# Kernel tuning notes

Measured on AMD Instinct MI355X. Metric: run time of the kernel, lower is better.

## Reference

```python
import jax, jax.numpy as jnp
import numpy as np

# ---- static structure (from LastFMModel source) ----
COUNTS = (50000, 80000, 10000)   # user, item, tag node counts
FEAT, HID, INTRA, INTER = 256, 128, 64, 128
E = 500000                        # edges per metapath hop
# hops listed leaf->target as (src_type, dst_type, edge_type)
MP_USER = [[(0, 1, 0), (1, 0, 1)],
           [(0, 1, 0), (1, 2, 2), (2, 1, 3), (1, 0, 1)],
           [(0, 0, 4)]]
MP_ITEM = [[(1, 0, 1), (0, 1, 0)],
           [(1, 2, 2), (2, 1, 3)],
           [(1, 0, 1), (0, 0, 4), (0, 1, 0)]]
# get_gcn_encoder: etype in {1,2,4} -> encoder 1, {0,3} -> encoder 2
GCN_GROUP = {0: 2, 1: 1, 2: 1, 3: 2, 4: 1}
OFFSETS = (0, COUNTS[0], COUNTS[0] + COUNTS[1])


def _gen_edges(mps, rng):
    rows = []
    for hops in mps:
        for (st, dt, et) in hops:
            rows.append(np.stack([rng.integers(0, COUNTS[st], E),
                                  rng.integers(0, COUNTS[dt], E)]))
    return jnp.asarray(np.stack(rows), jnp.int32)


def setup_inputs() -> dict:
    rng = np.random.default_rng(0)
    ks = jax.random.split(jax.random.key(0), 16)
    n_total = sum(COUNTS)
    s = 0.05
    d = {}
    d['features'] = jax.random.normal(ks[0], (n_total, FEAT), jnp.float32)
    d['edges_user'] = _gen_edges(MP_USER, rng)
    d['edges_item'] = _gen_edges(MP_ITEM, rng)
    d['perm_user'] = jnp.asarray(rng.permutation(COUNTS[0]), jnp.int32)
    d['perm_item'] = jnp.asarray(rng.permutation(COUNTS[1]), jnp.int32)
    d['W_type'] = jax.random.normal(ks[1], (3, FEAT, HID), jnp.float32) * s
    d['b_type'] = jnp.zeros((3, HID), jnp.float32)
    d['comp_vec'] = jax.random.normal(ks[2], (5, HID), jnp.float32) * s
    d['W_gcn'] = jax.random.normal(ks[3], (3, HID, HID), jnp.float32) * s
    d['b_gcn'] = jnp.zeros((3, HID), jnp.float32)
    d['fc_u'] = jax.random.normal(ks[4], (3, HID, INTRA), jnp.float32) * s
    d['fcr_u'] = jax.random.normal(ks[5], (3, INTRA, HID), jnp.float32) * s
    d['V_u'] = jax.random.normal(ks[6], (3 * INTRA, INTER), jnp.float32) * s
    d['Vr_u'] = jax.random.normal(ks[7], (INTER, 3 * INTRA), jnp.float32) * s
    d['fc_i'] = jax.random.normal(ks[8], (3, HID, INTRA), jnp.float32) * s
    d['fcr_i'] = jax.random.normal(ks[9], (3, INTRA, HID), jnp.float32) * s
    d['V_i'] = jax.random.normal(ks[10], (3 * INTRA, INTER), jnp.float32) * s
    d['Vr_i'] = jax.random.normal(ks[11], (INTER, 3 * INTRA), jnp.float32) * s
    return d


def _propagate(h_src, src, dst, etype, n_dst, comp_vec, W_gcn, b_gcn):
    # CompGCN composition (elementwise) + GraphConv norm='right' (in-degree mean)
    msg = h_src[src] * comp_vec[etype]                                  # [E, HID]
    agg = jax.ops.segment_sum(msg, dst, num_segments=n_dst)
    deg = jax.ops.segment_sum(jnp.ones_like(dst, jnp.float32), dst, num_segments=n_dst)
    h = agg / jnp.clip(deg, 1.0)[:, None]
    g = GCN_GROUP[etype]
    return h @ W_gcn[g] + b_gcn[g]


def _fusion(outs, fc, fcr, V, Vr):
    # AutoMvFusion: per-view intra projection, shared inter fusion,
    # reconstruction loss + pairwise view orthogonality loss
    z_list = [jnp.tanh(h @ fc[p]) for p, h in enumerate(outs)]          # [N, INTRA] each
    z = jnp.concatenate(z_list, axis=1)                                 # [N, 3*INTRA]
    fused = z @ V                                                       # [N, INTER]
    z_rec = fused @ Vr
    re = jnp.float32(0.0)
    for p, h in enumerate(outs):
        h_rec = z_rec[:, p * INTRA:(p + 1) * INTRA] @ fcr[p]
        re = re + jnp.mean((h_rec - h) ** 2)
    orth = jnp.float32(0.0)
    for p in range(3):
        for q in range(p + 1, 3):
            g = z_list[p].T @ z_list[q]                                 # [INTRA, INTRA]
            orth = orth + jnp.mean(g ** 2)
    return fused, re + orth


def _run_layer(mp_hops, edges, perm, t_feats, comp_vec, W_gcn, b_gcn, fc, fcr, V, Vr):
    k = 0
    outs = []
    for hops in mp_hops:
        h = t_feats[hops[0][0]]           # leaf-type transformed features
        for (st, dt, et) in hops:
            h = _propagate(h, edges[k, 0], edges[k, 1], et, COUNTS[dt],
                           comp_vec, W_gcn, b_gcn)
            k += 1
        outs.append(h[perm])              # new_index_arrangement reindex
    return _fusion(outs, fc, fcr, V, Vr)


def reference(features, edges_user, edges_item, perm_user, perm_item,
              W_type, b_type, comp_vec, W_gcn, b_gcn,
              fc_u, fcr_u, V_u, Vr_u, fc_i, fcr_i, V_i, Vr_i):
    # NodeTransform: per-type linear + activation (dropout off at eval)
    t_feats = [jax.nn.relu(features[OFFSETS[t]:OFFSETS[t] + COUNTS[t]] @ W_type[t] + b_type[t])
               for t in range(3)]
    h_user, loss_u = _run_layer(MP_USER, edges_user, perm_user, t_feats,
                                comp_vec, W_gcn, b_gcn, fc_u, fcr_u, V_u, Vr_u)
    h_item, loss_i = _run_layer(MP_ITEM, edges_item, perm_item, t_feats,
                                comp_vec, W_gcn, b_gcn, fc_i, fcr_i, V_i, Vr_i)
    return h_user, h_item, loss_u + loss_i
```

## Files before the change

### kernel.cpp

```cpp
#include <hip/hip_runtime.h>

typedef unsigned short u16;
typedef unsigned int   u32;

#define ACT_NONE 0
#define ACT_RELU 1
#define ACT_TANH 2

#define E_EDGES 500000
#define RP_STRIDE 80004
#define NCH 62
#define CH 8192
#define HSTRIDE 19456

using s8vec = __attribute__((ext_vector_type(8))) short;
using f4vec = __attribute__((ext_vector_type(4))) float;

__device__ __forceinline__ float bf2f(u16 u) {
  union { u32 b; float f; } v; v.b = ((u32)u) << 16; return v.f;
}
__device__ __forceinline__ u16 f2bf(float x) {
  union { float f; u32 b; } v; v.f = x;
  u32 r = v.b + 0x7fffu + ((v.b >> 16) & 1u);
  return (u16)(r >> 16);
}
__device__ __forceinline__ void acc8(float* acc, uint4 v) {
  union { u32 b; float f; } cv;
  cv.b = v.x << 16;         acc[0] += cv.f;
  cv.b = v.x & 0xffff0000u; acc[1] += cv.f;
  cv.b = v.y << 16;         acc[2] += cv.f;
  cv.b = v.y & 0xffff0000u; acc[3] += cv.f;
  cv.b = v.z << 16;         acc[4] += cv.f;
  cv.b = v.z & 0xffff0000u; acc[5] += cv.f;
  cv.b = v.w << 16;         acc[6] += cv.f;
  cv.b = v.w & 0xffff0000u; acc[7] += cv.f;
}

struct TJob { const float* src; u16* dst; const float* scale; int R; int C; };
struct TBatch { TJob j[24]; };
__global__ __launch_bounds__(256) void transpose_b_k(TBatch b) {
  TJob jb = b.j[blockIdx.y];
  int i = blockIdx.x * 256 + threadIdx.x;
  if (i >= jb.R * jb.C) return;
  int r = i / jb.C, c = i % jb.C;
  float v = jb.src[i];
  if (jb.scale) v *= jb.scale[r];
  jb.dst[(size_t)c * jb.R + r] = f2bf(v);
}

struct IBatch { const int* perm[2]; int* ip[2]; int n[2]; };
__global__ __launch_bounds__(256) void iperm_b_k(IBatch b) {
  int y = blockIdx.y;
  int i = blockIdx.x * 256 + threadIdx.x;
  if (i < b.n[y]) b.ip[y][b.perm[y][i]] = i;
}

struct CsrP { int n[14]; int sh[14]; int P[14]; };

__global__ __launch_bounds__(256) void csr_hist_k(
    const int* __restrict__ eu, const int* __restrict__ ei,
    int* __restrict__ hista, CsrP cp) {
  const int hop = blockIdx.y, chunk = blockIdx.x;
  const int P = cp.P[hop], sh = cp.sh[hop];
  __shared__ int hist[320];
  for (int i = threadIdx.x; i < P; i += 256) hist[i] = 0;
  __syncthreads();
  const int* edges = (hop < 7) ? eu : ei;
  const int h7 = (hop < 7) ? hop : hop - 7;
  const int* dstp = edges + (size_t)(h7 * 2 + 1) * E_EDGES;
  const int e0 = chunk * CH;
  const int e1 = min(E_EDGES, e0 + CH);
  for (int e = e0 + threadIdx.x * 4; e < e1; e += 1024) {
    int4 d4 = *(const int4*)(dstp + e);
    atomicAdd(&hist[d4.x >> sh], 1);
    atomicAdd(&hist[d4.y >> sh], 1);
    atomicAdd(&hist[d4.z >> sh], 1);
    atomicAdd(&hist[d4.w >> sh], 1);
  }
  __syncthreads();
  for (int i = threadIdx.x; i < P; i += 256)
    hista[(size_t)hop * HSTRIDE + i * NCH + chunk] = hist[i];
}

__global__ __launch_bounds__(256) void csr_scan_k(int* __restrict__ hista, CsrP cp) {
  const int hop = blockIdx.x;
  const int L = cp.P[hop] * NCH;
  int* a = hista + (size_t)hop * HSTRIDE;
  const int per = (L + 255) >> 8;
  const int lo = threadIdx.x * per;
  const int hi = min(L, lo + per);
  int s = 0;
  for (int i = lo; i < hi; ++i) s += a[i];
  __shared__ int lds[256];
  lds[threadIdx.x] = s;
  __syncthreads();
  for (int off = 1; off < 256; off <<= 1) {
    int v = (threadIdx.x >= off) ? lds[threadIdx.x - off] : 0;
    __syncthreads();
    lds[threadIdx.x] += v;
    __syncthreads();
  }
  int run = threadIdx.x ? lds[threadIdx.x - 1] : 0;
  for (int i = lo; i < hi; ++i) { int v = a[i]; a[i] = run; run += v; }
}

__global__ __launch_bounds__(256) void csr_scatter_k(
    const int* __restrict__ eu, const int* __restrict__ ei,
    const int* __restrict__ hista, u32* __restrict__ bp, CsrP cp) {
  const int hop = blockIdx.y, chunk = blockIdx.x;
  const int P = cp.P[hop], sh = cp.sh[hop];
  const u32 fm = (1u << sh) - 1u;
  __shared__ int cur[320];
  for (int i = threadIdx.x; i < P; i += 256)
    cur[i] = hista[(size_t)hop * HSTRIDE + i * NCH + chunk];
  __syncthreads();
  const int* edges = (hop < 7) ? eu : ei;
  const int h7 = (hop < 7) ? hop : hop - 7;
  const int* srcp = edges + (size_t)(h7 * 2) * E_EDGES;
  const int* dstp = srcp + E_EDGES;
  u32* b = bp + (size_t)hop * E_EDGES;
  const int e0 = chunk * CH;
  const int e1 = min(E_EDGES, e0 + CH);
  for (int e = e0 + threadIdx.x * 4; e < e1; e += 1024) {
    int4 d4 = *(const int4*)(dstp + e);
    int4 s4 = *(const int4*)(srcp + e);
    int dd[4] = {d4.x, d4.y, d4.z, d4.w};
    int ss[4] = {s4.x, s4.y, s4.z, s4.w};
#pragma unroll
    for (int j = 0; j < 4; ++j) {
      int pos = atomicAdd(&cur[dd[j] >> sh], 1);
      b[pos] = (u32)ss[j] | (((u32)dd[j] & fm) << 24);
    }
  }
}

__global__ __launch_bounds__(256) void csr_fine_k(
    const u32* __restrict__ bp, const int* __restrict__ hista,
    int* __restrict__ rowptrb, int* __restrict__ esrcb, CsrP cp) {
  const int hop = blockIdx.y, p = blockIdx.x;
  const int P = cp.P[hop];
  if (p >= P) return;
  const int n = cp.n[hop], sh = cp.sh[hop], W = 1 << sh;
  const int* fl = hista + (size_t)hop * HSTRIDE;
  const int beg = fl[p * NCH];
  const int end = (p + 1 < P) ? fl[(p + 1) * NCH] : E_EDGES;
  const int nb = min(W, n - p * W);
  const int tid = threadIdx.x;

  __shared__ int fh[256];
  __shared__ int sc[256];
  __shared__ int cur[256];
  fh[tid] = 0;
  __syncthreads();
  const u32* b = bp + (size_t)hop * E_EDGES;
  for (int i = beg + tid; i < end; i += 256)
    atomicAdd(&fh[b[i] >> 24], 1);
  __syncthreads();
  sc[tid] = fh[tid];
  __syncthreads();
  for (int off = 1; off < 256; off <<= 1) {
    int v = (tid >= off) ? sc[tid - off] : 0;
    __syncthreads();
    sc[tid] += v;
    __syncthreads();
  }
  const int excl = tid ? sc[tid - 1] : 0;
  int* rowptr = rowptrb + (size_t)hop * RP_STRIDE;
  if (tid < nb) rowptr[p * W + tid] = beg + excl;
  cur[tid] = beg + excl;
  if (p == P - 1 && tid == 0) rowptr[n] = E_EDGES;
  __syncthreads();
  int* esrc = esrcb + (size_t)hop * E_EDGES;
  for (int i = beg + tid; i < end; i += 256) {
    u32 v = b[i];
    int pos = atomicAdd(&cur[v >> 24], 1);
    esrc[pos] = (int)(v & 0xFFFFFFu);
  }
}

struct HopJob {
  const u16* h; const int* rowptr; const int* esrc;
  const u16* Bt; const float* bias; u16* out;
  const int* iperm; int n; int permout;
};
struct HopBatch { HopJob j[6]; };

__global__ __launch_bounds__(512) void hop_b_k(HopBatch batch) {
  const HopJob jb = batch.j[blockIdx.y];
  const int rbase = blockIdx.x * 128;
  if (rbase >= jb.n) return;

  __shared__ u16 bts[128 * 128];
  const int tid = threadIdx.x;
  for (int i = tid; i < 128 * 16; i += 512) {
    int nn = i >> 4, g = i & 15;
    int gs = (g & 8) | ((g ^ nn) & 7);
    *(uint4*)(&bts[nn * 128 + gs * 8]) = *(const uint4*)(jb.Bt + (size_t)nn * 128 + g * 8);
  }
  __syncthreads();

  const int wave = tid >> 6;
  const int lane = tid & 63;
  const int kgrp = lane >> 4;
  const int lid  = lane & 15;
  const int d = rbase + wave * 16 + lid;

  float a0[8] = {0,0,0,0,0,0,0,0}, a1[8] = {0,0,0,0,0,0,0,0};
  float a2[8] = {0,0,0,0,0,0,0,0}, a3[8] = {0,0,0,0,0,0,0,0};
  int s0 = 0, s1 = 0;
  if (d < jb.n) { s0 = jb.rowptr[d]; s1 = jb.rowptr[d + 1]; }
  const u16* hk = jb.h + kgrp * 8;
  int i = s0;
  for (; i + 3 < s1; i += 4) {
    int ea = jb.esrc[i], eb = jb.esrc[i + 1], ec = jb.esrc[i + 2], ed = jb.esrc[i + 3];
    const u16* ra = hk + (size_t)ea * 128;
    const u16* rb = hk + (size_t)eb * 128;
    const u16* rc = hk + (size_t)ec * 128;
    const u16* rd = hk + (size_t)ed * 128;
    uint4 va0 = *(const uint4*)(ra);      uint4 vb0 = *(const uint4*)(rb);
    uint4 vc0 = *(const uint4*)(rc);      uint4 vd0 = *(const uint4*)(rd);
    uint4 va1 = *(const uint4*)(ra + 32); uint4 vb1 = *(const uint4*)(rb + 32);
    uint4 vc1 = *(const uint4*)(rc + 32); uint4 vd1 = *(const uint4*)(rd + 32);
    uint4 va2 = *(const uint4*)(ra + 64); uint4 vb2 = *(const uint4*)(rb + 64);
    uint4 vc2 = *(const uint4*)(rc + 64); uint4 vd2 = *(const uint4*)(rd + 64);
    uint4 va3 = *(const uint4*)(ra + 96); uint4 vb3 = *(const uint4*)(rb + 96);
    uint4 vc3 = *(const uint4*)(rc + 96); uint4 vd3 = *(const uint4*)(rd + 96);
    acc8(a0, va0); acc8(a0, vb0); acc8(a0, vc0); acc8(a0, vd0);
    acc8(a1, va1); acc8(a1, vb1); acc8(a1, vc1); acc8(a1, vd1);
    acc8(a2, va2); acc8(a2, vb2); acc8(a2, vc2); acc8(a2, vd2);
    acc8(a3, va3); acc8(a3, vb3); acc8(a3, vc3); acc8(a3, vd3);
  }
  for (; i + 1 < s1; i += 2) {
    const u16* ra = hk + (size_t)jb.esrc[i] * 128;
    const u16* rb = hk + (size_t)jb.esrc[i + 1] * 128;
    uint4 va0 = *(const uint4*)(ra);      uint4 vb0 = *(const uint4*)(rb);
    uint4 va1 = *(const uint4*)(ra + 32); uint4 vb1 = *(const uint4*)(rb + 32);
    uint4 va2 = *(const uint4*)(ra + 64); uint4 vb2 = *(const uint4*)(rb + 64);
    uint4 va3 = *(const uint4*)(ra + 96); uint4 vb3 = *(const uint4*)(rb + 96);
    acc8(a0, va0); acc8(a1, va1); acc8(a2, va2); acc8(a3, va3);
    acc8(a0, vb0); acc8(a1, vb1); acc8(a2, vb2); acc8(a3, vb3);
  }
  if (i < s1) {
    const u16* ra = hk + (size_t)jb.esrc[i] * 128;
    acc8(a0, *(const uint4*)(ra));
    acc8(a1, *(const uint4*)(ra + 32));
    acc8(a2, *(const uint4*)(ra + 64));
    acc8(a3, *(const uint4*)(ra + 96));
  }
  const float rs = 1.0f / fmaxf((float)(s1 - s0), 1.0f);
  s8vec f0, f1, f2, f3;
#pragma unroll
  for (int j = 0; j < 8; ++j) f0[j] = (short)f2bf(a0[j] * rs);
#pragma unroll
  for (int j = 0; j < 8; ++j) f1[j] = (short)f2bf(a1[j] * rs);
#pragma unroll
  for (int j = 0; j < 8; ++j) f2[j] = (short)f2bf(a2[j] * rs);
#pragma unroll
  for (int j = 0; j < 8; ++j) f3[j] = (short)f2bf(a3[j] * rs);

#pragma unroll
  for (int t = 0; t < 8; ++t) {
    f4vec c = {0.f, 0.f, 0.f, 0.f};
    const int bn = t * 16 + lid;
    int g = kgrp;
    int gs = (g & 8) | ((g ^ bn) & 7);
    c = __builtin_amdgcn_mfma_f32_16x16x32_bf16(f0, *(const s8vec*)(&bts[bn * 128 + gs * 8]), c, 0, 0, 0);
    g = 4 + kgrp; gs = (g & 8) | ((g ^ bn) & 7);
    c = __builtin_amdgcn_mfma_f32_16x16x32_bf16(f1, *(const s8vec*)(&bts[bn * 128 + gs * 8]), c, 0, 0, 0);
    g = 8 + kgrp; gs = (g & 8) | ((g ^ bn) & 7);
    c = __builtin_amdgcn_mfma_f32_16x16x32_bf16(f2, *(const s8vec*)(&bts[bn * 128 + gs * 8]), c, 0, 0, 0);
    g = 12 + kgrp; gs = (g & 8) | ((g ^ bn) & 7);
    c = __builtin_amdgcn_mfma_f32_16x16x32_bf16(f3, *(const s8vec*)(&bts[bn * 128 + gs * 8]), c, 0, 0, 0);
    const int col = bn;
    const float bb = jb.bias[col];
#pragma unroll
    for (int j = 0; j < 4; ++j) {
      int r = rbase + wave * 16 + kgrp * 4 + j;
      if (r < jb.n) {
        float v = c[j] + bb;
        int ro = jb.permout ? jb.iperm[r] : r;
        jb.out[(size_t)ro * 128 + col] = f2bf(v);
      }
    }
  }
}

struct GemmJob {
  const void* A; const u16* Bt; const float* bias; void* C;
  const u16* target; float* loss; u16* Ct; int M;
};
struct GemmBatch { GemmJob j[3]; };

template <int K, int N, int ACT, int AMODE, bool CF32, bool SQDIFF, bool CTR>
__global__ __launch_bounds__(256) void gemm_b_k(
    GemmBatch batch, int ldA, int ldC, int ldCt) {
  static_assert(K % 32 == 0 && N % 16 == 0, "");
  const GemmJob jb = batch.j[blockIdx.y];
  const int rbase0 = blockIdx.x * 64;
  if (rbase0 >= jb.M) return;

  __shared__ u16 bts[N * K];
  __shared__ float red[4];

  const int tid = threadIdx.x;
  for (int i = tid; i < N * (K / 8); i += 256) {
    int n = i / (K / 8);
    int g = i % (K / 8);
    int gs = (g & ~7) | ((g ^ n) & 7);
    *(uint4*)(&bts[n * K + gs * 8]) = *(const uint4*)(jb.Bt + (size_t)n * K + g * 8);
  }
  __syncthreads();

  const int wave = tid >> 6;
  const int lane = tid & 63;
  const int kgrp = lane >> 4;
  const int rbase = rbase0 + wave * 16;
  const int rowA = rbase + (lane & 15);
  const bool av = rowA < jb.M;

  s8vec afr[K / 32];
  if constexpr (AMODE == 1) {
    const float* arow = (const float*)jb.A + (size_t)rowA * ldA;
#pragma unroll
    for (int kt = 0; kt < K / 32; ++kt) {
      s8vec fr = {0, 0, 0, 0, 0, 0, 0, 0};
      if (av) {
        const float* p = arow + kt * 32 + kgrp * 8;
        float4 fa = *(const float4*)(p);
        float4 fb = *(const float4*)(p + 4);
        fr[0] = (short)f2bf(fa.x); fr[1] = (short)f2bf(fa.y);
        fr[2] = (short)f2bf(fa.z); fr[3] = (short)f2bf(fa.w);
        fr[4] = (short)f2bf(fb.x); fr[5] = (short)f2bf(fb.y);
        fr[6] = (short)f2bf(fb.z); fr[7] = (short)f2bf(fb.w);
      }
      afr[kt] = fr;
    }
  } else {
    const u16* arow = (const u16*)jb.A + (size_t)rowA * ldA;
#pragma unroll
    for (int kt = 0; kt < K / 32; ++kt) {
      s8vec fr = {0, 0, 0, 0, 0, 0, 0, 0};
      if (av) fr = *(const s8vec*)(arow + kt * 32 + kgrp * 8);
      afr[kt] = fr;
    }
  }

  float sqsum = 0.0f;
#pragma unroll
  for (int t = 0; t < N / 16; ++t) {
    f4vec acc = {0.f, 0.f, 0.f, 0.f};
    const int bn = t * 16 + (lane & 15);
#pragma unroll
    for (int kt = 0; kt < K / 32; ++kt) {
      int g = kt * 4 + kgrp;
      int gs = (g & ~7) | ((g ^ bn) & 7);
      s8vec bfr = *(const s8vec*)(&bts[bn * K + gs * 8]);
      acc = __builtin_amdgcn_mfma_f32_16x16x32_bf16(afr[kt], bfr, acc, 0, 0, 0);
    }
    const int col = t * 16 + (lane & 15);
    float bb = jb.bias ? jb.bias[col] : 0.0f;
#pragma unroll
    for (int j = 0; j < 4; ++j) {
      int r = rbase + kgrp * 4 + j;
      if (r < jb.M) {
        float v = acc[j] + bb;
        if constexpr (ACT == ACT_RELU) v = fmaxf(v, 0.0f);
        if constexpr (ACT == ACT_TANH) v = tanhf(v);
        if constexpr (SQDIFF) {
          float dd = v - bf2f(jb.target[(size_t)r * N + col]);
          sqsum += dd * dd;
        } else if constexpr (CF32) {
          ((float*)jb.C)[(size_t)r * ldC + col] = v;
        } else {
          ((u16*)jb.C)[(size_t)r * ldC + col] = f2bf(v);
        }
        if constexpr (CTR) {
          jb.Ct[(size_t)col * ldCt + r] = f2bf(v);
        }
      }
    }
  }

  if constexpr (SQDIFF) {
#pragma unroll
    for (int off = 32; off > 0; off >>= 1) sqsum += __shfl_down(sqsum, off);
    if (lane == 0) red[wave] = sqsum;
    __syncthreads();
    if (tid == 0) atomicAdd(jb.loss, red[0] + red[1] + red[2] + red[3]);
  }
}

#define GRAM_NKB 40
__global__ __launch_bounds__(256) void gram_k(
    const u16* __restrict__ zt, int NP, float* __restrict__ G3) {
  const int pair = blockIdx.y;
  const int p = (pair == 2) ? 1 : 0;
  const int q = (pair == 0) ? 1 : 2;
  const int wave = threadIdx.x >> 6;
  const int lane = threadIdx.x & 63;
  const int kgrp = lane >> 4, lid = lane & 15;

  const int KC = (((NP + GRAM_NKB - 1) / GRAM_NKB) + 31) & ~31;
  const int kbeg = blockIdx.x * KC;
  const int kend = min(NP, kbeg + KC);

  const u16* arow = zt + (size_t)(p * 64 + wave * 16 + lid) * NP;
  const u16* brow0 = zt + (size_t)(q * 64 + 0 * 16 + lid) * NP;
  const u16* brow1 = zt + (size_t)(q * 64 + 1 * 16 + lid) * NP;
  const u16* brow2 = zt + (size_t)(q * 64 + 2 * 16 + lid) * NP;
  const u16* brow3 = zt + (size_t)(q * 64 + 3 * 16 + lid) * NP;

  f4vec acc0 = {0.f, 0.f, 0.f, 0.f};
  f4vec acc1 = {0.f, 0.f, 0.f, 0.f};
  f4vec acc2 = {0.f, 0.f, 0.f, 0.f};
  f4vec acc3 = {0.f, 0.f, 0.f, 0.f};

  for (int k0 = kbeg; k0 < kend; k0 += 32) {
    const int ko = k0 + kgrp * 8;
    s8vec af = *(const s8vec*)(arow + ko);
    s8vec b0 = *(const s8vec*)(brow0 + ko);
    s8vec b1 = *(const s8vec*)(brow1 + ko);
    s8vec b2 = *(const s8vec*)(brow2 + ko);
    s8vec b3 = *(const s8vec*)(brow3 + ko);
    acc0 = __builtin_amdgcn_mfma_f32_16x16x32_bf16(af, b0, acc0, 0, 0, 0);
    acc1 = __builtin_amdgcn_mfma_f32_16x16x32_bf16(af, b1, acc1, 0, 0, 0);
    acc2 = __builtin_amdgcn_mfma_f32_16x16x32_bf16(af, b2, acc2, 0, 0, 0);
    acc3 = __builtin_amdgcn_mfma_f32_16x16x32_bf16(af, b3, acc3, 0, 0, 0);
  }

  float* g = G3 + (size_t)pair * 4096;
  const int mrow = wave * 16 + kgrp * 4;
#pragma unroll
  for (int j = 0; j < 4; ++j) {
    atomicAdd(&g[(mrow + j) * 64 + 0 * 16 + lid], acc0[j]);
    atomicAdd(&g[(mrow + j) * 64 + 1 * 16 + lid], acc1[j]);
    atomicAdd(&g[(mrow + j) * 64 + 2 * 16 + lid], acc2[j]);
    atomicAdd(&g[(mrow + j) * 64 + 3 * 16 + lid], acc3[j]);
  }
}

__global__ __launch_bounds__(256) void loss_k(
    const float* __restrict__ G, const float* __restrict__ RE,
    float* __restrict__ out) {
  float s = 0.f;
  for (int i = threadIdx.x; i < 2 * 3 * 4096; i += 256) { float g = G[i]; s += g * g; }
#pragma unroll
  for (int off = 32; off > 0; off >>= 1) s += __shfl_down(s, off);
  __shared__ float red[4];
  int wave = threadIdx.x >> 6, lane = threadIdx.x & 63;
  if (lane == 0) red[wave] = s;
  __syncthreads();
  if (threadIdx.x == 0) {
    float orth = (red[0] + red[1] + red[2] + red[3]) / 4096.0f;
    float loss = orth + RE[0] / (50000.0f * 128.0f) + RE[1] / (80000.0f * 128.0f);
    out[0] = loss;
  }
}

static const int COUNTS_H[3] = {50000, 80000, 10000};
static const int OFFS_H[3]   = {0, 50000, 130000};
static const int GRP_H[5]    = {2, 1, 1, 2, 1};
static const int HOPN[14] = {80000, 50000, 80000, 10000, 80000, 50000, 50000,
                             50000, 80000, 10000, 80000, 50000, 50000, 80000};

extern "C" void kernel_launch(void* const* d_in, const int* in_sizes, int n_in,
                              void* d_out, int out_size, void* d_ws, size_t ws_size,
                              hipStream_t stream) {
  (void)in_sizes; (void)n_in; (void)out_size; (void)ws_size;

  const float* features = (const float*)d_in[0];
  const int* e_user   = (const int*)d_in[1];
  const int* e_item   = (const int*)d_in[2];
  const int* perm_u   = (const int*)d_in[3];
  const int* perm_i   = (const int*)d_in[4];
  const float* W_type = (const float*)d_in[5];
  const float* b_type = (const float*)d_in[6];
  const float* comp   = (const float*)d_in[7];
  const float* W_gcn  = (const float*)d_in[8];
  const float* b_gcn  = (const float*)d_in[9];
  const float* fc[2]  = {(const float*)d_in[10], (const float*)d_in[14]};
  const float* fcr[2] = {(const float*)d_in[11], (const float*)d_in[15]};
  const float* V[2]   = {(const float*)d_in[12], (const float*)d_in[16]};
  const float* Vr[2]  = {(const float*)d_in[13], (const float*)d_in[17]};
  float* out = (float*)d_out;

  char* base = (char*)d_ws;
  size_t off = 0;
  auto alloc = [&](size_t b) -> void* {
    void* p = base + off;
    off = (off + b + 255) & ~(size_t)255;
    return p;
  };
  u16* TF    = (u16*)alloc(140000ull * 128 * 2);
  u16* HB    = (u16*)alloc(330000ull * 128 * 2);
  u16* OUTSu = (u16*)alloc(3ull * 50000 * 128 * 2);
  u16* OUTSi = (u16*)alloc(3ull * 80000 * 128 * 2);
  int* HISTA    = (int*)alloc(14ull * HSTRIDE * 4);
  int* ROWPTR14 = (int*)alloc(14ull * RP_STRIDE * 4);
  int* ESRC14   = (int*)alloc(14ull * E_EDGES * 4);
  int* IPERM    = (int*)alloc(130000ull * 4);
  u16* WT_TYPE = (u16*)alloc(3ull * 128 * 256 * 2);
  u16* BT_HOP  = (u16*)alloc(5ull * 128 * 128 * 2);
  u16* FCT     = (u16*)alloc(6ull * 64 * 128 * 2);
  u16* VT      = (u16*)alloc(2ull * 128 * 192 * 2);
  u16* VRT     = (u16*)alloc(2ull * 192 * 128 * 2);
  u16* FCRT    = (u16*)alloc(6ull * 128 * 64 * 2);
  float* G   = (float*)alloc((2 * 3 * 4096 + 2) * 4);
  float* RE  = G + 2 * 3 * 4096;

  u32* BP   = (u32*)HB;
  u16* Z    = HB;
  u16* ZREC = HB + 80000ull * 192;
  u16* ZT   = (u16*)HISTA;

  const int hbrow[7] = {0, 80000, 160000, 170000, 220000, 230000, 280000};
  auto HBp = [&](int c) { return HB + (size_t)hbrow[c] * 128; };
  auto RP  = [&](int g) { return ROWPTR14 + (size_t)g * RP_STRIDE; };
  auto ES  = [&](int g) { return ESRC14 + (size_t)g * E_EDGES; };
  auto BT  = [&](int et) { return BT_HOP + (size_t)et * 128 * 128; };
  auto BG  = [&](int et) { return b_gcn + (size_t)GRP_H[et] * 128; };

  TBatch tb;
  int tj = 0;
  for (int t = 0; t < 3; ++t)
    tb.j[tj++] = {W_type + (size_t)t * 256 * 128, WT_TYPE + (size_t)t * 128 * 256, nullptr, 256, 128};
  for (int et = 0; et < 5; ++et)
    tb.j[tj++] = {W_gcn + (size_t)GRP_H[et] * 128 * 128, BT_HOP + (size_t)et * 128 * 128,
                  comp + (size_t)et * 128, 128, 128};
  for (int L = 0; L < 2; ++L)
    for (int p = 0; p < 3; ++p)
      tb.j[tj++] = {fc[L] + (size_t)p * 128 * 64, FCT + (size_t)(L * 3 + p) * 64 * 128, nullptr, 128, 64};
  for (int L = 0; L < 2; ++L)
    for (int p = 0; p < 3; ++p)
      tb.j[tj++] = {fcr[L] + (size_t)p * 64 * 128, FCRT + (size_t)(L * 3 + p) * 128 * 64, nullptr, 64, 128};
  for (int L = 0; L < 2; ++L)
    tb.j[tj++] = {V[L], VT + (size_t)L * 128 * 192, nullptr, 192, 128};
  for (int L = 0; L < 2; ++L)
    tb.j[tj++] = {Vr[L], VRT + (size_t)L * 192 * 128, nullptr, 128, 192};
  transpose_b_k<<<dim3(128, 24), 256, 0, stream>>>(tb);

  IBatch ib;
  ib.perm[0] = perm_u; ib.ip[0] = IPERM;          ib.n[0] = 50000;
  ib.perm[1] = perm_i; ib.ip[1] = IPERM + 50000;  ib.n[1] = 80000;
  iperm_b_k<<<dim3(313, 2), 256, 0, stream>>>(ib);

  CsrP cpp;
  for (int g = 0; g < 14; ++g) {
    cpp.n[g] = HOPN[g];
    cpp.sh[g] = (HOPN[g] <= 10000) ? 6 : 8;
    cpp.P[g] = (HOPN[g] + (1 << cpp.sh[g]) - 1) >> cpp.sh[g];
  }
  csr_hist_k<<<dim3(NCH, 14), 256, 0, stream>>>(e_user, e_item, HISTA, cpp);
  csr_scan_k<<<dim3(14), 256, 0, stream>>>(HISTA, cpp);
  csr_scatter_k<<<dim3(NCH, 14), 256, 0, stream>>>(e_user, e_item, HISTA, BP, cpp);
  csr_fine_k<<<dim3(313, 14), 256, 0, stream>>>(BP, HISTA, ROWPTR14, ESRC14, cpp);
  hipMemsetAsync(G, 0, (2 * 3 * 4096 + 2) * 4, stream);

  {
    GemmBatch nb;
    for (int t = 0; t < 3; ++t)
      nb.j[t] = {features + (size_t)OFFS_H[t] * 256, WT_TYPE + (size_t)t * 128 * 256,
                 b_type + (size_t)t * 128, TF + (size_t)OFFS_H[t] * 128,
                 nullptr, nullptr, nullptr, COUNTS_H[t]};
    gemm_b_k<256, 128, ACT_RELU, 1, false, false, false>
        <<<dim3(1250, 3), 256, 0, stream>>>(nb, 256, 128, 0);
  }

  const u16* TF0 = TF;
  const u16* TF1 = TF + 50000ull * 128;
  const int* IPu = IPERM;
  const int* IPi = IPERM + 50000;

  HopBatch L0, L1, L2, L3;
  L0.j[0] = {TF0, RP(0),  ES(0),  BT(0), BG(0), HBp(0), nullptr, 80000, 0};
  L0.j[1] = {TF0, RP(2),  ES(2),  BT(0), BG(0), HBp(1), nullptr, 80000, 0};
  L0.j[2] = {TF0, RP(6),  ES(6),  BT(4), BG(4), OUTSu + 2ull * 50000 * 128, IPu, 50000, 1};
  L0.j[3] = {TF1, RP(7),  ES(7),  BT(1), BG(1), HBp(3), nullptr, 50000, 0};
  L0.j[4] = {TF1, RP(9),  ES(9),  BT(2), BG(2), HBp(4), nullptr, 10000, 0};
  L0.j[5] = {TF1, RP(11), ES(11), BT(1), BG(1), HBp(5), nullptr, 50000, 0};
  L1.j[0] = {HBp(0), RP(1),  ES(1),  BT(1), BG(1), OUTSu, IPu, 50000, 1};
  L1.j[1] = {HBp(1), RP(3),  ES(3),  BT(2), BG(2), HBp(2), nullptr, 10000, 0};
  L1.j[2] = {HBp(3), RP(8),  ES(8),  BT(0), BG(0), OUTSi, IPi, 80000, 1};
  L1.j[3] = {HBp(4), RP(10), ES(10), BT(3), BG(3), OUTSi + 1ull * 80000 * 128, IPi, 80000, 1};
  L1.j[4] = {HBp(5), RP(12), ES(12), BT(4), BG(4), HBp(6), nullptr, 50000, 0};
  L1.j[5] = L1.j[4];
  L2.j[0] = {HBp(2), RP(4),  ES(4),  BT(3), BG(3), HBp(0), nullptr, 80000, 0};
  L2.j[1] = {HBp(6), RP(13), ES(13), BT(0), BG(0), OUTSi + 2ull * 80000 * 128, IPi, 80000, 1};
  L2.j[2] = L2.j[1]; L2.j[3] = L2.j[1]; L2.j[4] = L2.j[1]; L2.j[5] = L2.j[1];
  L3.j[0] = {HBp(0), RP(5), ES(5), BT(1), BG(1), OUTSu + 1ull * 50000 * 128, IPu, 50000, 1};
  L3.j[1] = L3.j[0]; L3.j[2] = L3.j[0]; L3.j[3] = L3.j[0]; L3.j[4] = L3.j[0]; L3.j[5] = L3.j[0];

  hop_b_k<<<dim3(625, 6), 512, 0, stream>>>(L0);
  hop_b_k<<<dim3(625, 5), 512, 0, stream>>>(L1);
  hop_b_k<<<dim3(625, 2), 512, 0, stream>>>(L2);
  hop_b_k<<<dim3(391, 1), 512, 0, stream>>>(L3);

  for (int L = 0; L < 2; ++L) {
    const int nL = L ? 80000 : 50000;
    const int NP = (nL + 31) & ~31;
    u16* OUTS_L = L ? OUTSi : OUTSu;
    const size_t pstride = (size_t)nL * 128;
    const dim3 gg((unsigned)((nL + 63) / 64));

    if (NP != nL)
      hipMemsetAsync(ZT, 0, (size_t)192 * NP * 2, stream);

    GemmBatch fb;
    for (int p = 0; p < 3; ++p)
      fb.j[p] = {OUTS_L + p * pstride, FCT + (size_t)(L * 3 + p) * 64 * 128, nullptr,
                 Z + p * 64, nullptr, nullptr, ZT + (size_t)p * 64 * NP, nL};
    gemm_b_k<128, 64, ACT_TANH, 0, false, false, true>
        <<<dim3(gg.x, 3), 256, 0, stream>>>(fb, 128, 192, NP);

    gram_k<<<dim3(GRAM_NKB, 3), 256, 0, stream>>>(ZT, NP, G + (size_t)L * 3 * 4096);

    float* fused = out + (L ? 6400000 : 0);
    GemmBatch vb;
    vb.j[0] = {Z, VT + (size_t)L * 128 * 192, nullptr, fused, nullptr, nullptr, nullptr, nL};
    vb.j[1] = vb.j[0]; vb.j[2] = vb.j[0];
    gemm_b_k<192, 128, ACT_NONE, 0, true, false, false>
        <<<dim3(gg.x, 1), 256, 0, stream>>>(vb, 192, 128, 0);

    GemmBatch rb;
    rb.j[0] = {fused, VRT + (size_t)L * 192 * 128, nullptr, ZREC, nullptr, nullptr, nullptr, nL};
    rb.j[1] = rb.j[0]; rb.j[2] = rb.j[0];
    gemm_b_k<128, 192, ACT_NONE, 1, false, false, false>
        <<<dim3(gg.x, 1), 256, 0, stream>>>(rb, 128, 192, 0);

    GemmBatch sb;
    for (int p = 0; p < 3; ++p)
      sb.j[p] = {ZREC + p * 64, FCRT + (size_t)(L * 3 + p) * 128 * 64, nullptr,
                 nullptr, OUTS_L + p * pstride, RE + L, nullptr, nL};
    gemm_b_k<64, 128, ACT_NONE, 0, false, true, false>
        <<<dim3(gg.x, 3), 256, 0, stream>>>(sb, 192, 0, 0);
  }

  loss_k<<<1, 256, 0, stream>>>(G, RE, out + 16640000);
}
```

Before: 1.119 ms.

## Sort destination rows by degree to balance hop aggregation, shrink hop blocks

Adds three kernels that build a per-hop permutation of destination rows bucketed by in-degree (counting sort over degrees capped at 63). The hop gather kernel now handles rows in that order, so the 16 lanes sharing a wave have similar edge counts and lanes spend less time idle on divergent loop trip counts. Output rows are remapped through the sort, and the hop block shrinks from 512 to 256 threads with 64 rows per block and more blocks. The cost is extra preprocessing launches, an indirect row lookup, and scattered output writes with less locality.

```diff
diff --git a/kernel.cpp b/kernel.cpp
--- a/kernel.cpp
+++ b/kernel.cpp
@@ -12,6 +12,9 @@
 #define NCH 62
 #define CH 8192
 #define HSTRIDE 19456
+#define DCH 2048
+#define DNCH 40
+#define DH_STRIDE (64 * DNCH)
 
 using s8vec = __attribute__((ext_vector_type(8))) short;
 using f4vec = __attribute__((ext_vector_type(4))) float;
@@ -178,21 +181,79 @@
   }
 }
 
+__global__ __launch_bounds__(256) void deg_hist_k(
+    const int* __restrict__ rowptrb, int* __restrict__ dh, CsrP cp) {
+  const int hop = blockIdx.y, ch = blockIdx.x;
+  const int n = cp.n[hop];
+  __shared__ int h[64];
+  if (threadIdx.x < 64) h[threadIdx.x] = 0;
+  __syncthreads();
+  const int* rp = rowptrb + (size_t)hop * RP_STRIDE;
+  const int d0 = ch * DCH;
+  const int d1 = min(n, d0 + DCH);
+  for (int d = d0 + threadIdx.x; d < d1; d += 256)
+    atomicAdd(&h[min(rp[d + 1] - rp[d], 63)], 1);
+  __syncthreads();
+  if (threadIdx.x < 64)
+    dh[(size_t)hop * DH_STRIDE + threadIdx.x * DNCH + ch] = h[threadIdx.x];
+}
+
+__global__ __launch_bounds__(256) void deg_scan_k(int* __restrict__ dh) {
+  int* a = dh + (size_t)blockIdx.x * DH_STRIDE;
+  const int L = DH_STRIDE;
+  const int per = (L + 255) >> 8;
+  const int lo = threadIdx.x * per;
+  const int hi = min(L, lo + per);
+  int s = 0;
+  for (int i = lo; i < hi; ++i) s += a[i];
+  __shared__ int lds[256];
+  lds[threadIdx.x] = s;
+  __syncthreads();
+  for (int off = 1; off < 256; off <<= 1) {
+    int v = (threadIdx.x >= off) ? lds[threadIdx.x - off] : 0;
+    __syncthreads();
+    lds[threadIdx.x] += v;
+    __syncthreads();
+  }
+  int run = threadIdx.x ? lds[threadIdx.x - 1] : 0;
+  for (int i = lo; i < hi; ++i) { int v = a[i]; a[i] = run; run += v; }
+}
+
+__global__ __launch_bounds__(256) void deg_scatter_k(
+    const int* __restrict__ rowptrb, const int* __restrict__ dh,
+    int* __restrict__ dsortb, CsrP cp) {
+  const int hop = blockIdx.y, ch = blockIdx.x;
+  const int n = cp.n[hop];
+  const int d0 = ch * DCH;
+  if (d0 >= n) return;
+  __shared__ int cur[64];
+  if (threadIdx.x < 64)
+    cur[threadIdx.x] = dh[(size_t)hop * DH_STRIDE + threadIdx.x * DNCH + ch];
+  __syncthreads();
+  const int* rp = rowptrb + (size_t)hop * RP_STRIDE;
+  int* ds = dsortb + (size_t)hop * RP_STRIDE;
+  const int d1 = min(n, d0 + DCH);
+  for (int d = d0 + threadIdx.x; d < d1; d += 256) {
+    int pos = atomicAdd(&cur[min(rp[d + 1] - rp[d], 63)], 1);
+    ds[pos] = d;
+  }
+}
+
 struct HopJob {
-  const u16* h; const int* rowptr; const int* esrc;
+  const u16* h; const int* rowptr; const int* esrc; const int* dsort;
   const u16* Bt; const float* bias; u16* out;
   const int* iperm; int n; int permout;
 };
 struct HopBatch { HopJob j[6]; };
 
-__global__ __launch_bounds__(512) void hop_b_k(HopBatch batch) {
+__global__ __launch_bounds__(256, 4) void hop_b_k(HopBatch batch) {
   const HopJob jb = batch.j[blockIdx.y];
-  const int rbase = blockIdx.x * 128;
+  const int rbase = blockIdx.x * 64;
   if (rbase >= jb.n) return;
 
   __shared__ u16 bts[128 * 128];
   const int tid = threadIdx.x;
-  for (int i = tid; i < 128 * 16; i += 512) {
+  for (int i = tid; i < 128 * 16; i += 256) {
     int nn = i >> 4, g = i & 15;
     int gs = (g & 8) | ((g ^ nn) & 7);
     *(uint4*)(&bts[nn * 128 + gs * 8]) = *(const uint4*)(jb.Bt + (size_t)nn * 128 + g * 8);
@@ -203,12 +264,16 @@
   const int lane = tid & 63;
   const int kgrp = lane >> 4;
   const int lid  = lane & 15;
-  const int d = rbase + wave * 16 + lid;
+  const int dv = rbase + wave * 16 + lid;
 
   float a0[8] = {0,0,0,0,0,0,0,0}, a1[8] = {0,0,0,0,0,0,0,0};
   float a2[8] = {0,0,0,0,0,0,0,0}, a3[8] = {0,0,0,0,0,0,0,0};
   int s0 = 0, s1 = 0;
-  if (d < jb.n) { s0 = jb.rowptr[d]; s1 = jb.rowptr[d + 1]; }
+  if (dv < jb.n) {
+    int d = jb.dsort[dv];
+    s0 = jb.rowptr[d];
+    s1 = jb.rowptr[d + 1];
+  }
   const u16* hk = jb.h + kgrp * 8;
   int i = s0;
   for (; i + 3 < s1; i += 4) {
@@ -258,6 +323,18 @@
 #pragma unroll
   for (int j = 0; j < 8; ++j) f3[j] = (short)f2bf(a3[j] * rs);
 
+  int rout[4];
+#pragma unroll
+  for (int j = 0; j < 4; ++j) {
+    int rv = rbase + wave * 16 + kgrp * 4 + j;
+    if (rv < jb.n) {
+      int rr = jb.dsort[rv];
+      rout[j] = jb.permout ? jb.iperm[rr] : rr;
+    } else {
+      rout[j] = -1;
+    }
+  }
+
 #pragma unroll
   for (int t = 0; t < 8; ++t) {
     f4vec c = {0.f, 0.f, 0.f, 0.f};
@@ -275,11 +352,9 @@
     const float bb = jb.bias[col];
 #pragma unroll
     for (int j = 0; j < 4; ++j) {
-      int r = rbase + wave * 16 + kgrp * 4 + j;
-      if (r < jb.n) {
+      if (rout[j] >= 0) {
         float v = c[j] + bb;
-        int ro = jb.permout ? jb.iperm[r] : r;
-        jb.out[(size_t)ro * 128 + col] = f2bf(v);
+        jb.out[(size_t)rout[j] * 128 + col] = f2bf(v);
       }
     }
   }
@@ -498,6 +573,8 @@
   int* HISTA    = (int*)alloc(14ull * HSTRIDE * 4);
   int* ROWPTR14 = (int*)alloc(14ull * RP_STRIDE * 4);
   int* ESRC14   = (int*)alloc(14ull * E_EDGES * 4);
+  int* DSORT14  = (int*)alloc(14ull * RP_STRIDE * 4);
+  int* DH       = (int*)alloc(14ull * DH_STRIDE * 4);
   int* IPERM    = (int*)alloc(130000ull * 4);
   u16* WT_TYPE = (u16*)alloc(3ull * 128 * 256 * 2);
   u16* BT_HOP  = (u16*)alloc(5ull * 128 * 128 * 2);
@@ -517,6 +594,7 @@
   auto HBp = [&](int c) { return HB + (size_t)hbrow[c] * 128; };
   auto RP  = [&](int g) { return ROWPTR14 + (size_t)g * RP_STRIDE; };
   auto ES  = [&](int g) { return ESRC14 + (size_t)g * E_EDGES; };
+  auto DS  = [&](int g) { return DSORT14 + (size_t)g * RP_STRIDE; };
   auto BT  = [&](int et) { return BT_HOP + (size_t)et * 128 * 128; };
   auto BG  = [&](int et) { return b_gcn + (size_t)GRP_H[et] * 128; };
 
@@ -554,6 +632,10 @@
   csr_scan_k<<<dim3(14), 256, 0, stream>>>(HISTA, cpp);
   csr_scatter_k<<<dim3(NCH, 14), 256, 0, stream>>>(e_user, e_item, HISTA, BP, cpp);
   csr_fine_k<<<dim3(313, 14), 256, 0, stream>>>(BP, HISTA, ROWPTR14, ESRC14, cpp);
+
+  deg_hist_k<<<dim3(DNCH, 14), 256, 0, stream>>>(ROWPTR14, DH, cpp);
+  deg_scan_k<<<dim3(14), 256, 0, stream>>>(DH);
+  deg_scatter_k<<<dim3(DNCH, 14), 256, 0, stream>>>(ROWPTR14, DH, DSORT14, cpp);
   hipMemsetAsync(G, 0, (2 * 3 * 4096 + 2) * 4, stream);
 
   {
@@ -572,28 +654,28 @@
   const int* IPi = IPERM + 50000;
 
   HopBatch L0, L1, L2, L3;
-  L0.j[0] = {TF0, RP(0),  ES(0),  BT(0), BG(0), HBp(0), nullptr, 80000, 0};
-  L0.j[1] = {TF0, RP(2),  ES(2),  BT(0), BG(0), HBp(1), nullptr, 80000, 0};
-  L0.j[2] = {TF0, RP(6),  ES(6),  BT(4), BG(4), OUTSu + 2ull * 50000 * 128, IPu, 50000, 1};
-  L0.j[3] = {TF1, RP(7),  ES(7),  BT(1), BG(1), HBp(3), nullptr, 50000, 0};
-  L0.j[4] = {TF1, RP(9),  ES(9),  BT(2), BG(2), HBp(4), nullptr, 10000, 0};
-  L0.j[5] = {TF1, RP(11), ES(11), BT(1), BG(1), HBp(5), nullptr, 50000, 0};
-  L1.j[0] = {HBp(0), RP(1),  ES(1),  BT(1), BG(1), OUTSu, IPu, 50000, 1};
-  L1.j[1] = {HBp(1), RP(3),  ES(3),  BT(2), BG(2), HBp(2), nullptr, 10000, 0};
-  L1.j[2] = {HBp(3), RP(8),  ES(8),  BT(0), BG(0), OUTSi, IPi, 80000, 1};
-  L1.j[3] = {HBp(4), RP(10), ES(10), BT(3), BG(3), OUTSi + 1ull * 80000 * 128, IPi, 80000, 1};
-  L1.j[4] = {HBp(5), RP(12), ES(12), BT(4), BG(4), HBp(6), nullptr, 50000, 0};
+  L0.j[0] = {TF0, RP(0),  ES(0),  DS(0),  BT(0), BG(0), HBp(0), nullptr, 80000, 0};
+  L0.j[1] = {TF0, RP(2),  ES(2),  DS(2),  BT(0), BG(0), HBp(1), nullptr, 80000, 0};
+  L0.j[2] = {TF0, RP(6),  ES(6),  DS(6),  BT(4), BG(4), OUTSu + 2ull * 50000 * 128, IPu, 50000, 1};
+  L0.j[3] = {TF1, RP(7),  ES(7),  DS(7),  BT(1), BG(1), HBp(3), nullptr, 50000, 0};
+  L0.j[4] = {TF1, RP(9),  ES(9),  DS(9),  BT(2), BG(2), HBp(4), nullptr, 10000, 0};
+  L0.j[5] = {TF1, RP(11), ES(11), DS(11), BT(1), BG(1), HBp(5), nullptr, 50000, 0};
+  L1.j[0] = {HBp(0), RP(1),  ES(1),  DS(1),  BT(1), BG(1), OUTSu, IPu, 50000, 1};
+  L1.j[1] = {HBp(1), RP(3),  ES(3),  DS(3),  BT(2), BG(2), HBp(2), nullptr, 10000, 0};
+  L1.j[2] = {HBp(3), RP(8),  ES(8),  DS(8),  BT(0), BG(0), OUTSi, IPi, 80000, 1};
+  L1.j[3] = {HBp(4), RP(10), ES(10), DS(10), BT(3), BG(3), OUTSi + 1ull * 80000 * 128, IPi, 80000, 1};
+  L1.j[4] = {HBp(5), RP(12), ES(12), DS(12), BT(4), BG(4), HBp(6), nullptr, 50000, 0};
   L1.j[5] = L1.j[4];
-  L2.j[0] = {HBp(2), RP(4),  ES(4),  BT(3), BG(3), HBp(0), nullptr, 80000, 0};
-  L2.j[1] = {HBp(6), RP(13), ES(13), BT(0), BG(0), OUTSi + 2ull * 80000 * 128, IPi, 80000, 1};
+  L2.j[0] = {HBp(2), RP(4),  ES(4),  DS(4),  BT(3), BG(3), HBp(0), nullptr, 80000, 0};
+  L2.j[1] = {HBp(6), RP(13), ES(13), DS(13), BT(0), BG(0), OUTSi + 2ull * 80000 * 128, IPi, 80000, 1};
   L2.j[2] = L2.j[1]; L2.j[3] = L2.j[1]; L2.j[4] = L2.j[1]; L2.j[5] = L2.j[1];
-  L3.j[0] = {HBp(0), RP(5), ES(5), BT(1), BG(1), OUTSu + 1ull * 50000 * 128, IPu, 50000, 1};
+  L3.j[0] = {HBp(0), RP(5), ES(5), DS(5), BT(1), BG(1), OUTSu + 1ull * 50000 * 128, IPu, 50000, 1};
   L3.j[1] = L3.j[0]; L3.j[2] = L3.j[0]; L3.j[3] = L3.j[0]; L3.j[4] = L3.j[0]; L3.j[5] = L3.j[0];
 
-  hop_b_k<<<dim3(625, 6), 512, 0, stream>>>(L0);
-  hop_b_k<<<dim3(625, 5), 512, 0, stream>>>(L1);
-  hop_b_k<<<dim3(625, 2), 512, 0, stream>>>(L2);
-  hop_b_k<<<dim3(391, 1), 512, 0, stream>>>(L3);
+  hop_b_k<<<dim3(1250, 6), 256, 0, stream>>>(L0);
+  hop_b_k<<<dim3(1250, 5), 256, 0, stream>>>(L1);
+  hop_b_k<<<dim3(1250, 2), 256, 0, stream>>>(L2);
+  hop_b_k<<<dim3(782, 1), 256, 0, stream>>>(L3);
 
   for (int L = 0; L < 2; ++L) {
     const int nL = L ? 80000 : 50000;
```

After: 1.118 ms. No clear change (-0.0%).
